# Kernel tuning notes

Measured on AMD Instinct MI355X. Metric: run time of the kernel, lower is better.

## Reference

```python
import jax, jax.numpy as jnp
import numpy as np

SEQ_LEN = 2048
D_MODEL = 1024
K = 32
B = 16
CP = K * (K + 1) // 2  # 528


def _spectral_filters(seq_len: int, k: int) -> np.ndarray:
    # Hankel matrix Z_ij = 2 / ((i+j)^3 - (i+j)), 1-indexed
    e = np.arange(1, seq_len + 1, dtype=np.float64)
    ipj = e[:, None] + e[None, :]
    Z = 2.0 / (ipj ** 3 - ipj)
    sigma, phi = np.linalg.eigh(Z)
    sk = np.clip(sigma[-k:], 1e-9, None)
    return (phi[:, -k:] * sk ** 0.25).astype(np.float32)


# static upper-triangular index pattern and sqrt(2) off-diagonal scaling
_IU0, _IU1 = np.triu_indices(K)
_SCALE = np.where(_IU0 == _IU1, 1.0, np.sqrt(2.0)).astype(np.float32)


def setup_inputs() -> dict:
    key = jax.random.key(0)
    ks = jax.random.split(key, 8)
    filters = jnp.asarray(_spectral_filters(SEQ_LEN, K))
    x = jax.random.normal(ks[0], (B, SEQ_LEN, D_MODEL), dtype=jnp.float32)
    pre_w = jax.random.normal(ks[1], (SEQ_LEN, D_MODEL), dtype=jnp.float32) / np.sqrt(D_MODEL)
    pre_b = jnp.zeros((SEQ_LEN,), dtype=jnp.float32)
    qp_w = jax.random.normal(ks[2], (CP, K), dtype=jnp.float32) / np.sqrt(K)
    qp_b = jnp.zeros((CP,), dtype=jnp.float32)
    o_w = jax.random.normal(ks[3], (D_MODEL, CP), dtype=jnp.float32) / np.sqrt(CP)
    o_b = jnp.zeros((D_MODEL,), dtype=jnp.float32)
    decay = jnp.ones((SEQ_LEN,), dtype=jnp.float32)
    return {
        'x': x,
        'pre_w': pre_w, 'pre_b': pre_b,
        'q_filters': filters,          # learnable copy
        'k_filters': filters,          # fixed buffer copy
        'qp_w': qp_w, 'qp_b': qp_b,
        'o_w': o_w, 'o_b': o_b,
        'decay': decay,
    }


def reference(x, pre_w, pre_b, q_filters, k_filters, qp_w, qp_b, o_w, o_b, decay):
    # pre_proj: (B,T,d_model) -> (B,T,seq_len)
    x_proj = x @ pre_w.T + pre_b
    # spectral projections onto top-K filters: (B,T,K)
    Q = jnp.einsum('bti,ik->btk', x_proj, q_filters)
    Q = Q @ qp_w.T + qp_b                      # (B,T,CP)
    V = jnp.einsum('bti,ik->btk', x_proj, k_filters)
    # symmetric outer product compressed to upper triangle, off-diag * sqrt(2)
    iu0 = jnp.asarray(_IU0)
    iu1 = jnp.asarray(_IU1)
    scale = jnp.asarray(_SCALE)
    Z = V[..., iu0] * V[..., iu1] * scale      # (B,T,CP), avoids (B,T,K,K)
    Z = Z * decay[None, :, None]
    H = jnp.cumsum(Z, axis=1)                  # causal state accumulation
    Y = Q * H
    return Y @ o_w.T + o_b                     # (B,T,d_model)
```

## Files before the change

### kernel.cpp

```cpp
#include <hip/hip_runtime.h>
#include <hip/hip_bf16.h>
#include <math.h>

#define T_SEQ   2048
#define DM      1024
#define KF      32
#define BATCH   16
#define CPDIM   528
#define KPAD    544
#define YSTR    552
#define QVSTR   36
#define MROWS   (BATCH * T_SEQ)
#define NCHUNK  32
#define TCHUNK  64

typedef __bf16 bf16x8 __attribute__((ext_vector_type(8)));
typedef float f32x4 __attribute__((ext_vector_type(4)));
typedef unsigned uint2v __attribute__((ext_vector_type(2)));

__device__ __forceinline__ unsigned packsplit(float v) {
  unsigned u = __float_as_uint(v);
  unsigned h = (u + 0x7fffu + ((u >> 16) & 1u)) & 0xffff0000u;
  float rr = v - __uint_as_float(h);
  return h | (__float_as_uint(rr) >> 16);
}

__device__ __forceinline__ unsigned short f2bf(float f) {
  unsigned u = __float_as_uint(f);
  return (unsigned short)((u + 0x7fffu + ((u >> 16) & 1u)) >> 16);
}
__device__ __forceinline__ float bf2f(unsigned short h) {
  return __uint_as_float((unsigned)h << 16);
}

__device__ __forceinline__ void gload16(const void* g, void* l) {
  __builtin_amdgcn_global_load_lds(
      (const __attribute__((address_space(1))) unsigned*)g,
      (__attribute__((address_space(3))) unsigned*)l, 16, 0, 0);
}

__global__ __launch_bounds__(256) void k_fold_part(const float* __restrict__ pre_w,
                                                   const float* __restrict__ qf,
                                                   const float* __restrict__ kfil,
                                                   float* __restrict__ Wp) {
  const int sc = blockIdx.x;
  const int it = blockIdx.y;
  const int s0 = sc * 64, i0 = it * 64;
  const int tid = threadIdx.x;
  __shared__ float fs[64][64];
  __shared__ float ps[64][64];
  for (int idx = tid; idx < 4096; idx += 256) {
    const int s = idx >> 6, c = idx & 63;
    fs[s][c] = (c < KF) ? qf[(s0 + s) * KF + c] : kfil[(s0 + s) * KF + c - KF];
    ps[s][c] = pre_w[(size_t)(s0 + s) * DM + i0 + c];
  }
  __syncthreads();
  const int i = tid & 63;
  const int kb = tid >> 6;
  float acc[16] = {};
  for (int s = 0; s < 64; ++s) {
    const float pv = ps[s][i];
    const float4 f0 = *reinterpret_cast<const float4*>(&fs[s][kb * 16 + 0]);
    const float4 f1 = *reinterpret_cast<const float4*>(&fs[s][kb * 16 + 4]);
    const float4 f2 = *reinterpret_cast<const float4*>(&fs[s][kb * 16 + 8]);
    const float4 f3 = *reinterpret_cast<const float4*>(&fs[s][kb * 16 + 12]);
    acc[0]  = fmaf(pv, f0.x, acc[0]);  acc[1]  = fmaf(pv, f0.y, acc[1]);
    acc[2]  = fmaf(pv, f0.z, acc[2]);  acc[3]  = fmaf(pv, f0.w, acc[3]);
    acc[4]  = fmaf(pv, f1.x, acc[4]);  acc[5]  = fmaf(pv, f1.y, acc[5]);
    acc[6]  = fmaf(pv, f1.z, acc[6]);  acc[7]  = fmaf(pv, f1.w, acc[7]);
    acc[8]  = fmaf(pv, f2.x, acc[8]);  acc[9]  = fmaf(pv, f2.y, acc[9]);
    acc[10] = fmaf(pv, f2.z, acc[10]); acc[11] = fmaf(pv, f2.w, acc[11]);
    acc[12] = fmaf(pv, f3.x, acc[12]); acc[13] = fmaf(pv, f3.y, acc[13]);
    acc[14] = fmaf(pv, f3.z, acc[14]); acc[15] = fmaf(pv, f3.w, acc[15]);
  }
#pragma unroll
  for (int j = 0; j < 16; ++j)
    Wp[((size_t)sc * 64 + kb * 16 + j) * DM + i0 + i] = acc[j];
}

__global__ __launch_bounds__(256) void k_foldred_bias(const float* __restrict__ Wp,
                                                      const float* __restrict__ pre_b,
                                                      const float* __restrict__ qf,
                                                      const float* __restrict__ kfil,
                                                      unsigned short* __restrict__ Wt_hi,
                                                      unsigned short* __restrict__ Wt_lo,
                                                      float* __restrict__ bias64) {
  if (blockIdx.x == 256) {
    __shared__ float part[4][64];
    const int k = threadIdx.x & 63;
    const int q = threadIdx.x >> 6;
    float acc = 0.f;
    for (int s = q * 512; s < (q + 1) * 512; ++s) {
      const float fv = (k < KF) ? qf[s * KF + k] : kfil[s * KF + k - KF];
      acc = fmaf(pre_b[s], fv, acc);
    }
    part[q][k] = acc;
    __syncthreads();
    if (threadIdx.x < 64)
      bias64[threadIdx.x] = part[0][k] + part[1][k] + part[2][k] + part[3][k];
    return;
  }
  const int idx = blockIdx.x * 256 + threadIdx.x;
  float acc = 0.f;
#pragma unroll
  for (int sc = 0; sc < NCHUNK; ++sc)
    acc += Wp[(size_t)sc * 64 * DM + idx];
  const unsigned pk = packsplit(acc);
  Wt_hi[idx] = (unsigned short)(pk >> 16);
  Wt_lo[idx] = (unsigned short)(pk & 0xffffu);
}

__global__ __launch_bounds__(256) void k_q0v_cs(const float* __restrict__ x,
                                                const unsigned short* __restrict__ Wt_hi,
                                                const unsigned short* __restrict__ Wt_lo,
                                                const float* __restrict__ bias64,
                                                const float* __restrict__ decay,
                                                float* __restrict__ Q0V,
                                                float* __restrict__ S) {
  __shared__ float Xs[2][64 * 32];
  __shared__ unsigned short Wh[2][64 * 32];
  __shared__ unsigned short Wl[2][64 * 32];
  __shared__ float vs2[64 * 32];
  __shared__ float dec2[64];
  const int tid = threadIdx.x;
  const int m0 = blockIdx.x * 64;
  const int w = tid >> 6, l = tid & 63;
  const int g = l >> 4, r = l & 15;

  f32x4 acc[4] = {};

  auto stage = [&](int buf, int k0) {
#pragma unroll
    for (int q = 0; q < 2; ++q) {
      const int c = q * 256 + tid;
      const int row = c >> 3, sl = c & 7;
      const int col4 = (sl ^ (row & 7)) * 4;
      gload16(&x[(size_t)(m0 + row) * DM + k0 + col4], &Xs[buf][c * 4]);
    }
    {
      const int row = tid >> 2, sl = tid & 3;
      const int colh = (sl ^ ((row >> 1) & 3)) * 8;
      gload16(&Wt_hi[(size_t)row * DM + k0 + colh], &Wh[buf][tid * 8]);
      gload16(&Wt_lo[(size_t)row * DM + k0 + colh], &Wl[buf][tid * 8]);
    }
  };

  if (tid < 64) dec2[tid] = decay[(m0 & 2047) + tid];

  stage(0, 0);
  for (int it = 0; it < DM / 32; ++it) {
    const int cur = it & 1;
    __syncthreads();
    if (it + 1 < DM / 32) stage(cur ^ 1, (it + 1) * 32);

    const int arow = w * 16 + r;
    const int sx = (2 * g) ^ (arow & 7);
    const int sy = (2 * g + 1) ^ (arow & 7);
    const f32x4 pX = *reinterpret_cast<const f32x4*>(&Xs[cur][arow * 32 + sx * 4]);
    const f32x4 pY = *reinterpret_cast<const f32x4*>(&Xs[cur][arow * 32 + sy * 4]);
    unsigned pk[8];
#pragma unroll
    for (int e = 0; e < 4; ++e) { pk[e] = packsplit(pX[e]); pk[4 + e] = packsplit(pY[e]); }
    union { unsigned u[4]; bf16x8 v; } ah, al;
#pragma unroll
    for (int j = 0; j < 4; ++j) {
      ah.u[j] = (pk[2 * j] >> 16) | (pk[2 * j + 1] & 0xffff0000u);
      al.u[j] = (pk[2 * j] & 0xffffu) | (pk[2 * j + 1] << 16);
    }

    bf16x8 bh[4], bl[4];
#pragma unroll
    for (int n = 0; n < 4; ++n) {
      const int brow = n * 16 + r;
      const int bs = g ^ ((brow >> 1) & 3);
      const int off = brow * 32 + bs * 8;
      bh[n] = *reinterpret_cast<const bf16x8*>(&Wh[cur][off]);
      bl[n] = *reinterpret_cast<const bf16x8*>(&Wl[cur][off]);
    }
#pragma unroll
    for (int n = 0; n < 4; ++n) {
      acc[n] = __builtin_amdgcn_mfma_f32_16x16x32_bf16(bh[n], ah.v, acc[n], 0, 0, 0);
      acc[n] = __builtin_amdgcn_mfma_f32_16x16x32_bf16(bh[n], al.v, acc[n], 0, 0, 0);
      acc[n] = __builtin_amdgcn_mfma_f32_16x16x32_bf16(bl[n], ah.v, acc[n], 0, 0, 0);
    }
  }

  const int trow = w * 16 + r;
  const int row_o = m0 + trow;
#pragma unroll
  for (int n = 0; n < 4; ++n) {
    const int col_o = n * 16 + g * 4;
    const float4 bb = *reinterpret_cast<const float4*>(&bias64[col_o]);
    float4 v;
    v.x = acc[n][0] + bb.x; v.y = acc[n][1] + bb.y;
    v.z = acc[n][2] + bb.z; v.w = acc[n][3] + bb.w;
    *reinterpret_cast<float4*>(&Q0V[(size_t)row_o * 64 + col_o]) = v;
    if (n >= 2)
      *reinterpret_cast<float4*>(&vs2[trow * 32 + (n - 2) * 16 + g * 4]) = v;
  }
  __syncthreads();

  const int b = m0 >> 11, ch = (m0 & 2047) >> 6;
#pragma unroll
  for (int pass = 0; pass < 3; ++pass) {
    const int c = tid + pass * 256;
    if (c < CPDIM) {
      int i = 0, rem = c;
      while (rem >= KF - i) { rem -= KF - i; ++i; }
      const int j = i + rem;
      const float sc = (i == j) ? 1.0f : 1.41421356237309515f;
      float h = 0.f;
#pragma unroll 4
      for (int t = 0; t < TCHUNK; ++t)
        h = fmaf(vs2[t * KF + i] * vs2[t * KF + j], dec2[t], h);
      S[(size_t)(b * NCHUNK + ch) * CPDIM + c] = h * sc;
    }
  }
}

__global__ __launch_bounds__(576) void k_scanchunks(float* __restrict__ S) {
  const int b = blockIdx.x;
  const int c = threadIdx.x;
  if (c >= CPDIM) return;
  float v[NCHUNK];
#pragma unroll
  for (int ch = 0; ch < NCHUNK; ++ch)
    v[ch] = S[(size_t)(b * NCHUNK + ch) * CPDIM + c];
  float run = 0.f;
#pragma unroll
  for (int ch = 0; ch < NCHUNK; ++ch) {
    S[(size_t)(b * NCHUNK + ch) * CPDIM + c] = run;
    run += v[ch];
  }
}

#define NB_OWB  (DM * KPAD / 256)
#define NB_QPW  (KPAD * KF / 256)
__global__ __launch_bounds__(256) void k_prep(const float* __restrict__ ow,
                                              const float* __restrict__ qp_w,
                                              const float* __restrict__ qp_b,
                                              unsigned short* __restrict__ owb,
                                              unsigned short* __restrict__ qpw_hi,
                                              unsigned short* __restrict__ qpw_lo,
                                              float* __restrict__ qpb_pad) {
  const int bx = blockIdx.x;
  if (bx < NB_OWB) {
    const int idx = bx * 256 + threadIdx.x;
    const int n = idx / KPAD, k = idx - n * KPAD;
    owb[idx] = (k < CPDIM) ? f2bf(ow[(size_t)n * CPDIM + k]) : (unsigned short)0;
  } else if (bx < NB_OWB + NB_QPW) {
    const int idx = (bx - NB_OWB) * 256 + threadIdx.x;
    const int c = idx >> 5;
    unsigned pk = 0;
    if (c < CPDIM) pk = packsplit(qp_w[idx]);
    qpw_hi[idx] = (unsigned short)(pk >> 16);
    qpw_lo[idx] = (unsigned short)(pk & 0xffffu);
  } else {
    for (int c = threadIdx.x; c < KPAD; c += 256)
      qpb_pad[c] = (c < CPDIM) ? qp_b[c] : 0.f;
  }
}

__global__ __launch_bounds__(512, 2) void k_out_fused(const float* __restrict__ Q0V,
                                                      const float* __restrict__ S,
                                                      const unsigned short* __restrict__ qpw_hi,
                                                      const unsigned short* __restrict__ qpw_lo,
                                                      const float* __restrict__ qpb_pad,
                                                      const float* __restrict__ decay,
                                                      const unsigned short* __restrict__ owb,
                                                      const float* __restrict__ ob,
                                                      float* __restrict__ out) {
  __shared__ float qs[64 * QVSTR];
  __shared__ float vs[64 * QVSTR];
  __shared__ float dec[64];
  __shared__ unsigned short Ylds[64 * YSTR];
  const int tid = threadIdx.x;
  const int m0 = blockIdx.x * 64;
  const int b = m0 >> 11, ch = (m0 & 2047) >> 6;
  const int t0 = m0 & 2047;
  const int wv = tid >> 6, l = tid & 63;
  const int g = l >> 4, r = l & 15;

#pragma unroll
  for (int ii = 0; ii < 2; ++ii) {
    const int idx = ii * 512 + tid;
    const int row = idx >> 4, c4 = idx & 15;
    const float4 v = *reinterpret_cast<const float4*>(&Q0V[(size_t)(m0 + row) * 64 + c4 * 4]);
    float* dst = (c4 < 8) ? &qs[row * QVSTR + c4 * 4] : &vs[row * QVSTR + (c4 - 8) * 4];
    *reinterpret_cast<float4*>(dst) = v;
  }
  if (tid < 64) dec[tid] = decay[t0 + tid];
  __syncthreads();

  {
    bf16x8 qah[4], qal[4];
#pragma unroll
    for (int m = 0; m < 4; ++m) {
      const int t = m * 16 + r;
      const f32x4 x0 = *reinterpret_cast<const f32x4*>(&qs[t * QVSTR + g * 8]);
      const f32x4 x1 = *reinterpret_cast<const f32x4*>(&qs[t * QVSTR + g * 8 + 4]);
      unsigned pk[8];
#pragma unroll
      for (int e = 0; e < 4; ++e) { pk[e] = packsplit(x0[e]); pk[4 + e] = packsplit(x1[e]); }
      union { unsigned u[4]; bf16x8 v; } hh, ll;
#pragma unroll
      for (int j = 0; j < 4; ++j) {
        hh.u[j] = (pk[2 * j] >> 16) | (pk[2 * j + 1] & 0xffff0000u);
        ll.u[j] = (pk[2 * j] & 0xffffu) | (pk[2 * j + 1] << 16);
      }
      qah[m] = hh.v; qal[m] = ll.v;
    }
    for (int nt = wv; nt < KPAD / 16; nt += 8) {
      const int crow = nt * 16 + r;
      const bf16x8 bh = *reinterpret_cast<const bf16x8*>(&qpw_hi[crow * KF + g * 8]);
      const bf16x8 bl = *reinterpret_cast<const bf16x8*>(&qpw_lo[crow * KF + g * 8]);
      const int cbase = nt * 16 + g * 4;
      const float4 qb4 = *reinterpret_cast<const float4*>(&qpb_pad[cbase]);
      f32x4 a[4];
#pragma unroll
      for (int m = 0; m < 4; ++m) { a[m][0] = qb4.x; a[m][1] = qb4.y; a[m][2] = qb4.z; a[m][3] = qb4.w; }
#pragma unroll
      for (int m = 0; m < 4; ++m) {
        a[m] = __builtin_amdgcn_mfma_f32_16x16x32_bf16(bh, qah[m], a[m], 0, 0, 0);
        a[m] = __builtin_amdgcn_mfma_f32_16x16x32_bf16(bh, qal[m], a[m], 0, 0, 0);
        a[m] = __builtin_amdgcn_mfma_f32_16x16x32_bf16(bl, qah[m], a[m], 0, 0, 0);
      }
#pragma unroll
      for (int m = 0; m < 4; ++m) {
        const int t = m * 16 + r;
        union { unsigned short s[4]; unsigned u[2]; } pk4;
#pragma unroll
        for (int j = 0; j < 4; ++j) pk4.s[j] = f2bf(a[m][j]);
        *reinterpret_cast<uint2v*>(&Ylds[t * YSTR + cbase]) = uint2v{pk4.u[0], pk4.u[1]};
      }
    }
  }
  __syncthreads();

#pragma unroll
  for (int pass = 0; pass < 2; ++pass) {
    const int c = tid + pass * 512;
    if (c < CPDIM) {
      int i = 0, rem = c;
      while (rem >= KF - i) { rem -= KF - i; ++i; }
      const int j = i + rem;
      const float sc = (i == j) ? 1.0f : 1.41421356237309515f;
      float h = S[(size_t)(b * NCHUNK + ch) * CPDIM + c];
      for (int t = 0; t < TCHUNK; ++t) {
        h = fmaf(vs[t * QVSTR + i] * vs[t * QVSTR + j] * sc, dec[t], h);
        const float qv = bf2f(Ylds[t * YSTR + c]);
        Ylds[t * YSTR + c] = f2bf(qv * h);
      }
    }
  }
  __syncthreads();

  f32x4 acc[4][8] = {};
  bf16x8 bA[8], bB[8];

  auto loadB = [&](bf16x8 (&dst)[8], int ks) {
    const int kh = ks * 32 + g * 8;
#pragma unroll
    for (int n = 0; n < 8; ++n)
      dst[n] = *reinterpret_cast<const bf16x8*>(&owb[(size_t)(wv * 128 + n * 16 + r) * KPAD + kh]);
  };
  auto step = [&](bf16x8 (&bcur)[8], int ks) {
    const int kh = ks * 32 + g * 8;
    bf16x8 af[4];
#pragma unroll
    for (int m = 0; m < 4; ++m)
      af[m] = *reinterpret_cast<const bf16x8*>(&Ylds[(m * 16 + r) * YSTR + kh]);
#pragma unroll
    for (int m = 0; m < 4; ++m)
#pragma unroll
      for (int n = 0; n < 8; ++n)
        acc[m][n] = __builtin_amdgcn_mfma_f32_16x16x32_bf16(bcur[n], af[m], acc[m][n], 0, 0, 0);
  };

  loadB(bA, 0);
  for (int ks = 0; ks < 16; ks += 2) {
    loadB(bB, ks + 1);
    step(bA, ks);
    loadB(bA, ks + 2);
    step(bB, ks + 1);
  }
  step(bA, 16);

#pragma unroll
  for (int m = 0; m < 4; ++m) {
    const int row_o = m0 + m * 16 + r;
#pragma unroll
    for (int n = 0; n < 8; ++n) {
      const int col_o = wv * 128 + n * 16 + g * 4;
      const float4 bb = *reinterpret_cast<const float4*>(&ob[col_o]);
      float4 v;
      v.x = acc[m][n][0] + bb.x; v.y = acc[m][n][1] + bb.y;
      v.z = acc[m][n][2] + bb.z; v.w = acc[m][n][3] + bb.w;
      *reinterpret_cast<float4*>(&out[(size_t)row_o * DM + col_o]) = v;
    }
  }
}

extern "C" void kernel_launch(void* const* d_in, const int* in_sizes, int n_in,
                              void* d_out, int out_size, void* d_ws, size_t ws_size,
                              hipStream_t stream) {
  const float* x      = (const float*)d_in[0];
  const float* pre_w  = (const float*)d_in[1];
  const float* pre_b  = (const float*)d_in[2];
  const float* q_filt = (const float*)d_in[3];
  const float* k_filt = (const float*)d_in[4];
  const float* qp_w   = (const float*)d_in[5];
  const float* qp_b   = (const float*)d_in[6];
  const float* o_w    = (const float*)d_in[7];
  const float* o_b    = (const float*)d_in[8];
  const float* decay  = (const float*)d_in[9];
  float* out = (float*)d_out;

  char* ws = (char*)d_ws;
  unsigned short* Wt_hi = (unsigned short*)(ws);
  unsigned short* Wt_lo = (unsigned short*)(ws + 131072);
  float*    bias64 = (float*)(ws + 262144);
  float*    Q0V    = (float*)(ws + 262400);
  float*    S      = (float*)(ws + 8651008);
  unsigned short* owb = (unsigned short*)(ws + 9732352);
  unsigned short* qpw_hi = (unsigned short*)(ws + 10846464);
  unsigned short* qpw_lo = (unsigned short*)(ws + 10881280);
  float*    qpb_pad = (float*)(ws + 10916096);
  float*    Wp     = (float*)(ws + 16777216);

  k_fold_part<<<dim3(NCHUNK, 16), dim3(256), 0, stream>>>(pre_w, q_filt, k_filt, Wp);
  k_foldred_bias<<<dim3(257), dim3(256), 0, stream>>>(Wp, pre_b, q_filt, k_filt, Wt_hi, Wt_lo, bias64);
  k_q0v_cs<<<dim3(MROWS / 64), dim3(256), 0, stream>>>(x, Wt_hi, Wt_lo, bias64, decay, Q0V, S);
  k_scanchunks<<<dim3(BATCH), dim3(576), 0, stream>>>(S);
  k_prep<<<dim3(NB_OWB + NB_QPW + 1), dim3(256), 0, stream>>>(o_w, qp_w, qp_b, owb, qpw_hi, qpw_lo, qpb_pad);
  k_out_fused<<<dim3(MROWS / 64), dim3(512), 0, stream>>>(Q0V, S, qpw_hi, qpw_lo, qpb_pad, decay, owb, o_b, out);
}
```

Measured before the change: 198.5 us.

## Triple-buffer projection loads and widen output kernel to 1024 threads

The x·W projection kernel moves from double to triple buffering, with explicit vmcnt waits and raw barriers, so two stages of global loads stay in flight while each stage computes. The fused output kernel now runs 1024 threads per block. Each wave computes a 64-column slice of the output GEMM with fewer accumulators, the scan uses one thread per compressed channel, and Q is read straight from global memory instead of being staged in LDS. This is meant to hide load latency and raise parallelism per block, at the cost of a hand-tuned wait count, no prefetch of the o_w loads, and launch bounds that ask for 4 blocks of 1024 threads.

```diff
diff --git a/kernel.cpp b/kernel.cpp
--- a/kernel.cpp
+++ b/kernel.cpp
@@ -117,9 +117,9 @@
                                                 const float* __restrict__ decay,
                                                 float* __restrict__ Q0V,
                                                 float* __restrict__ S) {
-  __shared__ float Xs[2][64 * 32];
-  __shared__ unsigned short Wh[2][64 * 32];
-  __shared__ unsigned short Wl[2][64 * 32];
+  __shared__ float Xs[3][64 * 32];
+  __shared__ unsigned short Wh[3][64 * 32];
+  __shared__ unsigned short Wl[3][64 * 32];
   __shared__ float vs2[64 * 32];
   __shared__ float dec2[64];
   const int tid = threadIdx.x;
@@ -145,14 +145,7 @@
     }
   };
 
-  if (tid < 64) dec2[tid] = decay[(m0 & 2047) + tid];
-
-  stage(0, 0);
-  for (int it = 0; it < DM / 32; ++it) {
-    const int cur = it & 1;
-    __syncthreads();
-    if (it + 1 < DM / 32) stage(cur ^ 1, (it + 1) * 32);
-
+  auto compute = [&](int cur) {
     const int arow = w * 16 + r;
     const int sx = (2 * g) ^ (arow & 7);
     const int sy = (2 * g + 1) ^ (arow & 7);
@@ -167,7 +160,6 @@
       ah.u[j] = (pk[2 * j] >> 16) | (pk[2 * j + 1] & 0xffff0000u);
       al.u[j] = (pk[2 * j] & 0xffffu) | (pk[2 * j + 1] << 16);
     }
-
     bf16x8 bh[4], bl[4];
 #pragma unroll
     for (int n = 0; n < 4; ++n) {
@@ -183,7 +175,32 @@
       acc[n] = __builtin_amdgcn_mfma_f32_16x16x32_bf16(bh[n], al.v, acc[n], 0, 0, 0);
       acc[n] = __builtin_amdgcn_mfma_f32_16x16x32_bf16(bl[n], ah.v, acc[n], 0, 0, 0);
     }
-  }
+  };
+
+  if (tid < 64) dec2[tid] = decay[(m0 & 2047) + tid];
+
+  stage(0, 0);
+  stage(1, 32);
+
+  for (int base = 0; base < 30; base += 3) {
+#pragma unroll
+    for (int sub = 0; sub < 3; ++sub) {
+      const int it = base + sub;
+      asm volatile("s_waitcnt vmcnt(4)" ::: "memory");
+      __builtin_amdgcn_s_barrier();
+      __builtin_amdgcn_sched_barrier(0);
+      stage((sub + 2) % 3, (it + 2) * 32);
+      compute(sub);
+    }
+  }
+  asm volatile("s_waitcnt vmcnt(4)" ::: "memory");
+  __builtin_amdgcn_s_barrier();
+  __builtin_amdgcn_sched_barrier(0);
+  compute(0);
+  asm volatile("s_waitcnt vmcnt(0)" ::: "memory");
+  __builtin_amdgcn_s_barrier();
+  __builtin_amdgcn_sched_barrier(0);
+  compute(1);
 
   const int trow = w * 16 + r;
   const int row_o = m0 + trow;
@@ -261,16 +278,15 @@
   }
 }
 
-__global__ __launch_bounds__(512, 2) void k_out_fused(const float* __restrict__ Q0V,
-                                                      const float* __restrict__ S,
-                                                      const unsigned short* __restrict__ qpw_hi,
-                                                      const unsigned short* __restrict__ qpw_lo,
-                                                      const float* __restrict__ qpb_pad,
-                                                      const float* __restrict__ decay,
-                                                      const unsigned short* __restrict__ owb,
-                                                      const float* __restrict__ ob,
-                                                      float* __restrict__ out) {
-  __shared__ float qs[64 * QVSTR];
+__global__ __launch_bounds__(1024, 4) void k_out_fused(const float* __restrict__ Q0V,
+                                                       const float* __restrict__ S,
+                                                       const unsigned short* __restrict__ qpw_hi,
+                                                       const unsigned short* __restrict__ qpw_lo,
+                                                       const float* __restrict__ qpb_pad,
+                                                       const float* __restrict__ decay,
+                                                       const unsigned short* __restrict__ owb,
+                                                       const float* __restrict__ ob,
+                                                       float* __restrict__ out) {
   __shared__ float vs[64 * QVSTR];
   __shared__ float dec[64];
   __shared__ unsigned short Ylds[64 * YSTR];
@@ -281,24 +297,20 @@
   const int wv = tid >> 6, l = tid & 63;
   const int g = l >> 4, r = l & 15;
 
-#pragma unroll
-  for (int ii = 0; ii < 2; ++ii) {
-    const int idx = ii * 512 + tid;
-    const int row = idx >> 4, c4 = idx & 15;
-    const float4 v = *reinterpret_cast<const float4*>(&Q0V[(size_t)(m0 + row) * 64 + c4 * 4]);
-    float* dst = (c4 < 8) ? &qs[row * QVSTR + c4 * 4] : &vs[row * QVSTR + (c4 - 8) * 4];
-    *reinterpret_cast<float4*>(dst) = v;
+  if (tid < 512) {
+    const int row = tid >> 3, c4 = tid & 7;
+    const float4 v = *reinterpret_cast<const float4*>(&Q0V[(size_t)(m0 + row) * 64 + 32 + c4 * 4]);
+    *reinterpret_cast<float4*>(&vs[row * QVSTR + c4 * 4]) = v;
   }
   if (tid < 64) dec[tid] = decay[t0 + tid];
-  __syncthreads();
 
   {
     bf16x8 qah[4], qal[4];
 #pragma unroll
     for (int m = 0; m < 4; ++m) {
       const int t = m * 16 + r;
-      const f32x4 x0 = *reinterpret_cast<const f32x4*>(&qs[t * QVSTR + g * 8]);
-      const f32x4 x1 = *reinterpret_cast<const f32x4*>(&qs[t * QVSTR + g * 8 + 4]);
+      const f32x4 x0 = *reinterpret_cast<const f32x4*>(&Q0V[(size_t)(m0 + t) * 64 + g * 8]);
+      const f32x4 x1 = *reinterpret_cast<const f32x4*>(&Q0V[(size_t)(m0 + t) * 64 + g * 8 + 4]);
       unsigned pk[8];
 #pragma unroll
       for (int e = 0; e < 4; ++e) { pk[e] = packsplit(x0[e]); pk[4 + e] = packsplit(x1[e]); }
@@ -310,7 +322,7 @@
       }
       qah[m] = hh.v; qal[m] = ll.v;
     }
-    for (int nt = wv; nt < KPAD / 16; nt += 8) {
+    for (int nt = wv; nt < KPAD / 16; nt += 16) {
       const int crow = nt * 16 + r;
       const bf16x8 bh = *reinterpret_cast<const bf16x8*>(&qpw_hi[crow * KF + g * 8]);
       const bf16x8 bl = *reinterpret_cast<const bf16x8*>(&qpw_lo[crow * KF + g * 8]);
@@ -337,61 +349,44 @@
   }
   __syncthreads();
 
-#pragma unroll
-  for (int pass = 0; pass < 2; ++pass) {
-    const int c = tid + pass * 512;
-    if (c < CPDIM) {
-      int i = 0, rem = c;
-      while (rem >= KF - i) { rem -= KF - i; ++i; }
-      const int j = i + rem;
-      const float sc = (i == j) ? 1.0f : 1.41421356237309515f;
-      float h = S[(size_t)(b * NCHUNK + ch) * CPDIM + c];
-      for (int t = 0; t < TCHUNK; ++t) {
-        h = fmaf(vs[t * QVSTR + i] * vs[t * QVSTR + j] * sc, dec[t], h);
-        const float qv = bf2f(Ylds[t * YSTR + c]);
-        Ylds[t * YSTR + c] = f2bf(qv * h);
-      }
+  if (tid < CPDIM) {
+    const int c = tid;
+    int i = 0, rem = c;
+    while (rem >= KF - i) { rem -= KF - i; ++i; }
+    const int j = i + rem;
+    const float sc = (i == j) ? 1.0f : 1.41421356237309515f;
+    float h = S[(size_t)(b * NCHUNK + ch) * CPDIM + c];
+    for (int t = 0; t < TCHUNK; ++t) {
+      h = fmaf(vs[t * QVSTR + i] * vs[t * QVSTR + j] * sc, dec[t], h);
+      const float qv = bf2f(Ylds[t * YSTR + c]);
+      Ylds[t * YSTR + c] = f2bf(qv * h);
     }
   }
   __syncthreads();
 
-  f32x4 acc[4][8] = {};
-  bf16x8 bA[8], bB[8];
-
-  auto loadB = [&](bf16x8 (&dst)[8], int ks) {
+  f32x4 acc[4][4] = {};
+  for (int ks = 0; ks <= 16; ++ks) {
     const int kh = ks * 32 + g * 8;
-#pragma unroll
-    for (int n = 0; n < 8; ++n)
-      dst[n] = *reinterpret_cast<const bf16x8*>(&owb[(size_t)(wv * 128 + n * 16 + r) * KPAD + kh]);
-  };
-  auto step = [&](bf16x8 (&bcur)[8], int ks) {
-    const int kh = ks * 32 + g * 8;
-    bf16x8 af[4];
+    bf16x8 bf4[4], af[4];
+#pragma unroll
+    for (int n = 0; n < 4; ++n)
+      bf4[n] = *reinterpret_cast<const bf16x8*>(&owb[(size_t)(wv * 64 + n * 16 + r) * KPAD + kh]);
 #pragma unroll
     for (int m = 0; m < 4; ++m)
       af[m] = *reinterpret_cast<const bf16x8*>(&Ylds[(m * 16 + r) * YSTR + kh]);
 #pragma unroll
     for (int m = 0; m < 4; ++m)
 #pragma unroll
-      for (int n = 0; n < 8; ++n)
-        acc[m][n] = __builtin_amdgcn_mfma_f32_16x16x32_bf16(bcur[n], af[m], acc[m][n], 0, 0, 0);
-  };
-
-  loadB(bA, 0);
-  for (int ks = 0; ks < 16; ks += 2) {
-    loadB(bB, ks + 1);
-    step(bA, ks);
-    loadB(bA, ks + 2);
-    step(bB, ks + 1);
-  }
-  step(bA, 16);
+      for (int n = 0; n < 4; ++n)
+        acc[m][n] = __builtin_amdgcn_mfma_f32_16x16x32_bf16(bf4[n], af[m], acc[m][n], 0, 0, 0);
+  }
 
 #pragma unroll
   for (int m = 0; m < 4; ++m) {
     const int row_o = m0 + m * 16 + r;
 #pragma unroll
-    for (int n = 0; n < 8; ++n) {
-      const int col_o = wv * 128 + n * 16 + g * 4;
+    for (int n = 0; n < 4; ++n) {
+      const int col_o = wv * 64 + n * 16 + g * 4;
       const float4 bb = *reinterpret_cast<const float4*>(&ob[col_o]);
       float4 v;
       v.x = acc[m][n][0] + bb.x; v.y = acc[m][n][1] + bb.y;
@@ -433,5 +428,5 @@
   k_q0v_cs<<<dim3(MROWS / 64), dim3(256), 0, stream>>>(x, Wt_hi, Wt_lo, bias64, decay, Q0V, S);
   k_scanchunks<<<dim3(BATCH), dim3(576), 0, stream>>>(S);
   k_prep<<<dim3(NB_OWB + NB_QPW + 1), dim3(256), 0, stream>>>(o_w, qp_w, qp_b, owb, qpw_hi, qpw_lo, qpb_pad);
-  k_out_fused<<<dim3(MROWS / 64), dim3(512), 0, stream>>>(Q0V, S, qpw_hi, qpw_lo, qpb_pad, decay, owb, o_b, out);
-}
+  k_out_fused<<<dim3(MROWS / 64), dim3(1024), 0, stream>>>(Q0V, S, qpw_hi, qpw_lo, qpb_pad, decay, owb, o_b, out);
+}
```

Result: faster. 184.6 us (-7.0%).
